# Kernel optimization log

Measured on AMD Instinct MI355X. Metric: run time of the kernel, lower is better.

Reference implementation:

```python
import jax, jax.numpy as jnp
import numpy as np

BS, SEQ, D_IN, D_OUT = 4, 1024, 1024, 1024
N_SKILLS, RANK = 8, 4
SCALING = 1.0  # lora_alpha / rank, folded into one constant
NEG_INF = -1e38


def setup_inputs() -> dict:
    key = jax.random.key(0)
    ks = jax.random.split(key, 5)
    x = jax.random.normal(ks[0], (BS, SEQ, D_IN), jnp.float32)
    phi = jax.random.normal(ks[1], (D_IN, N_SKILLS), jnp.float32) * 0.02
    lora_a = jax.random.normal(ks[2], (N_SKILLS, D_IN, RANK), jnp.float32) * 0.02
    lora_b = jax.random.normal(ks[3], (N_SKILLS, RANK, D_OUT), jnp.float32) * 0.02
    W = jax.random.normal(ks[4], (D_OUT, D_IN), jnp.float32) * 0.02
    b = jnp.zeros((D_OUT,), jnp.float32)
    # left-padded sequences with an instruction prefix right after the padding
    pad_len = np.array([100, 0, 250, 50])
    inst_len = 300
    pad = np.zeros((BS, SEQ), np.int32)
    inst = np.zeros((BS, SEQ), np.int32)
    for i in range(BS):
        pad[i, pad_len[i]:] = 1
        inst[i, pad_len[i]:pad_len[i] + inst_len] = 1
    return {"x": x, "phi": phi, "lora_a": lora_a, "lora_b": lora_b,
            "W": W, "b": b,
            "inst_mask": jnp.asarray(inst), "pad_mask": jnp.asarray(pad)}


def _causal_prefix_mask(inst_mask, pad_mask):
    # faithful port of create_causal_prefix_mask (padding_side='left')
    bs, seq = inst_mask.shape
    first_one = jnp.argmax(inst_mask, axis=1, keepdims=True)          # [b,1]
    n_ones = jnp.sum(inst_mask, axis=1, keepdims=True)                # [b,1]
    thresh = first_one + n_ones                                       # last_one_idx + 1
    exp = jnp.broadcast_to(thresh, (bs, seq))                         # [b,s]
    inv = jnp.maximum(seq - exp - jnp.arange(seq)[None, :], 0)[:, ::-1]
    m = (exp + inv) * pad_mask                                        # [b,s]
    m3 = m[:, :, None] * pad_mask[:, None, :]                         # [b,s,s]
    ar = jnp.arange(seq)[None, None, :]
    return ar < m3                                                    # bool [b,s,s]


def reference(x, phi, lora_a, lora_b, W, b, inst_mask, pad_mask):
    # router: mixing logits per token per skill
    mw = jnp.einsum('bsd,dn->bsn', x, phi)                            # [b,s,k]
    cm = _causal_prefix_mask(inst_mask, pad_mask)                     # [b,s,s]
    padf = pad_mask.astype(x.dtype)
    # expand over attended positions p, mask, softmax over p
    logits = jnp.where(cm[..., None], mw[:, :, None, :], NEG_INF)     # [b,s,p,k]
    logits = jnp.transpose(logits, (0, 3, 1, 2))                      # [b,k,s,p]
    D = jax.nn.softmax(logits, axis=-1)
    D = D * padf[:, None, :, None]                                    # zero padded query rows
    # token mixing: contract over source tokens (last axis of D)
    input_mixed = jnp.einsum('bsd,bkps->bkpd', x, D)                  # [b,k,s,d]
    # per-skill LoRA (n_splits == 1, q squeezed)
    ar_r = jnp.einsum('bksd,kdr->bskr', input_mixed, lora_a)          # [b,s,k,r]
    ad = jnp.einsum('bskr,krd->bskd', ar_r, lora_b)                   # [b,s,k,d_out]
    # softmax-weighted combine over skills
    C = jax.nn.softmax(mw, axis=-1)
    adapter_out = jnp.einsum('bsk,bskd->bsd', C, ad) * SCALING
    base = jnp.einsum('bsd,od->bso', x, W) + b
    return base + adapter_out
```

## Files before the change

kernel.cpp:

```cpp
#include <hip/hip_runtime.h>
#include <hip/hip_bf16.h>
#include <cstdint>

#define SEQ   1024
#define DOUT  1024
#define KDIM  1024
#define MTOT  4096

typedef __bf16 bf16x8 __attribute__((ext_vector_type(8)));
typedef float  f32x4  __attribute__((ext_vector_type(4)));

__device__ inline unsigned short f2bf(float f) {
  union { float f; unsigned u; } a; a.f = f;
  unsigned r = a.u + 0x7fff + ((a.u >> 16) & 1);
  return (unsigned short)(r >> 16);
}

__device__ inline void gl16(const void* g, void* l) {
  __builtin_amdgcn_global_load_lds((__attribute__((address_space(1))) void*)g,
                                   (__attribute__((address_space(3))) void*)l, 16, 0, 0);
}

__global__ __launch_bounds__(256) void k_prep(const float4* __restrict__ x, ushort4* __restrict__ xb,
                                              const float* __restrict__ phi, const float* __restrict__ la,
                                              unsigned short* __restrict__ Wc) {
  int blk = blockIdx.x, tid = threadIdx.x;
  if (blk < 4096) {
    int i = blk * 256 + tid;
    float4 v = x[i];
    ushort4 o; o.x = f2bf(v.x); o.y = f2bf(v.y); o.z = f2bf(v.z); o.w = f2bf(v.w);
    xb[i] = o;
  } else {
    int i = (blk - 4096) * 256 + tid;
    int row = 1024 + (i >> 10), d = i & 1023;
    float v;
    if (row < 1032)       v = phi[d * 8 + (row - 1024)];
    else if (row < 1064)  { int kr = row - 1032; v = la[(kr >> 2) * 4096 + d * 4 + (kr & 3)]; }
    else                  v = 0.f;
    Wc[(size_t)row * 1024 + d] = f2bf(v);
  }
}

__global__ __launch_bounds__(256) void k_mwz(const unsigned short* __restrict__ xb,
                                             const unsigned short* __restrict__ Wc0,
                                             const float* __restrict__ W, const float* __restrict__ lb,
                                             const int* __restrict__ inst,
                                             unsigned short* __restrict__ Wc, unsigned short* __restrict__ B2T,
                                             int* __restrict__ thr, float* __restrict__ mwzP) {
  __shared__ unsigned short As[64 * 32];
  __shared__ unsigned short Bs[48 * 32];
  int blk = blockIdx.x, t = threadIdx.x;
  if (blk >= 256) {
    if (blk < 4352) {
      size_t i = (size_t)(blk - 256) * 256 + t;
      Wc[i] = f2bf(W[i]);
    } else if (blk < 4480) {
      int i = (blk - 4352) * 256 + t;
      int n = i >> 5, kr = i & 31;
      B2T[i] = f2bf(lb[kr * 1024 + n]);
    } else {
      int b = t >> 6, lane = t & 63;
      int fo = 1 << 30, no = 0;
#pragma unroll
      for (int j = 0; j < 16; ++j) {
        int p = j * 64 + lane;
        int iv = inst[b * SEQ + p];
        if (iv > 0) fo = min(fo, p);
        no += iv;
      }
#pragma unroll
      for (int d = 1; d < 64; d <<= 1) { fo = min(fo, __shfl_xor(fo, d)); no += __shfl_xor(no, d); }
      if (lane == 0) thr[b] = (no > 0) ? fo + no : 0;
    }
    return;
  }
  int bm = blk & 63, ks = blk >> 6;
  int wave = t >> 6, lane = t & 63;
  int quad = lane >> 4, lr = lane & 15;
  f32x4 acc[3];
#pragma unroll
  for (int i = 0; i < 3; ++i) acc[i] = (f32x4){0.f, 0.f, 0.f, 0.f};
  const unsigned short* aG = xb + (size_t)bm * 64 * KDIM + ks * 256;
  const unsigned short* bG = Wc0 + (size_t)1024 * KDIM + ks * 256;
  int r0 = t >> 2, c0 = (t & 3) * 8;
  for (int kb = 0; kb < 256; kb += 32) {
    __syncthreads();
    gl16(aG + (size_t)r0 * KDIM + kb + c0, &As[wave * 512]);
    if (t < 192) gl16(bG + (size_t)r0 * KDIM + kb + c0, &Bs[wave * 512]);
    __syncthreads();
    bf16x8 af = *(const bf16x8*)&As[(wave * 16 + lr) * 32 + quad * 8];
#pragma unroll
    for (int ni = 0; ni < 3; ++ni) {
      bf16x8 bfr = *(const bf16x8*)&Bs[(ni * 16 + lr) * 32 + quad * 8];
      acc[ni] = __builtin_amdgcn_mfma_f32_16x16x32_bf16(af, bfr, acc[ni], 0, 0, 0);
    }
  }
#pragma unroll
  for (int ni = 0; ni < 3; ++ni) {
    int c = ni * 16 + lr;
#pragma unroll
    for (int rg = 0; rg < 4; ++rg) {
      int row = bm * 64 + wave * 16 + quad * 4 + rg;
      if (c < 40) mwzP[(size_t)(ks * 40 + c) * MTOT + row] = acc[ni][rg];
    }
  }
}

__global__ __launch_bounds__(1024) void k_scan_gate(const float* __restrict__ mwzP,
                                                    const int* __restrict__ pad, const int* __restrict__ thr,
                                                    unsigned short* __restrict__ gb) {
  int b = blockIdx.x, c = blockIdx.y;
  int tid = threadIdx.x, wv = tid >> 6, lane = tid & 63;
  __shared__ float wsz[16], wsp[16];
  __shared__ float sv, spc;
  int q = b * SEQ + tid;
  float pm = (float)pad[q];
  float z = 0.f;
#pragma unroll
  for (int s = 0; s < 4; ++s) z += mwzP[(size_t)(s * 40 + 8 + c) * MTOT + q];
  z *= pm;
  float vz = z, vp = pm;
#pragma unroll
  for (int d = 1; d < 64; d <<= 1) {
    float oz = __shfl_up(vz, d), op = __shfl_up(vp, d);
    if (lane >= d) { vz += oz; vp += op; }
  }
  if (lane == 63) { wsz[wv] = vz; wsp[wv] = vp; }
  __syncthreads();
  if (wv == 0 && lane < 16) {
    float oz = wsz[lane], op = wsp[lane], sz = oz, sp = op;
#pragma unroll
    for (int d = 1; d < 16; d <<= 1) {
      float tz = __shfl_up(sz, d), tp = __shfl_up(sp, d);
      if (lane >= d) { sz += tz; sp += tp; }
    }
    wsz[lane] = sz - oz; wsp[lane] = sp - op;
  }
  __syncthreads();
  vz += wsz[wv]; vp += wsp[wv];
  int th = thr[b];
  if (th > 0 && tid == th - 1) { sv = vz; spc = vp; }
  __syncthreads();
  unsigned short o = 0;
  if (pm != 0.f) {
    bool own = (tid + 1 >= th);
    float Tv  = own ? vz : sv;
    float cnt = own ? vp : spc;
    float C[8], mx = -1e30f;
#pragma unroll
    for (int k = 0; k < 8; ++k) {
      float m = 0.f;
#pragma unroll
      for (int s = 0; s < 4; ++s) m += mwzP[(size_t)(s * 40 + k) * MTOT + q];
      C[k] = m; mx = fmaxf(mx, m);
    }
    float sm = 0.f;
#pragma unroll
    for (int k = 0; k < 8; ++k) { C[k] = __expf(C[k] - mx); sm += C[k]; }
    o = f2bf(C[c >> 2] * Tv / (sm * cnt));
  }
  gb[(size_t)q * 32 + c] = o;
}

__global__ __launch_bounds__(256) void k_gemm(const unsigned short* __restrict__ A,
                                              const unsigned short* __restrict__ Wc,
                                              const unsigned short* __restrict__ gb,
                                              const unsigned short* __restrict__ B2T,
                                              float* __restrict__ out,
                                              const float* __restrict__ bias) {
  __shared__ __align__(16) unsigned short As[2][128 * 64];
  __shared__ __align__(16) unsigned short Bs[2][64 * 64];
  int bm = blockIdx.x, bn = blockIdx.y;
  int t = threadIdx.x;
  int wave = t >> 6, lane = t & 63;
  int wr = wave >> 1, wc = wave & 1;
  int quad = lane >> 4, lr = lane & 15;
  f32x4 acc[4][2];
#pragma unroll
  for (int i = 0; i < 4; i++)
#pragma unroll
    for (int j = 0; j < 2; j++) acc[i][j] = (f32x4){0.f, 0.f, 0.f, 0.f};

  {
    bf16x8 ga[4], gBf[2];
#pragma unroll
    for (int mi = 0; mi < 4; mi++)
      ga[mi] = *(const bf16x8*)(gb + (size_t)(bm * 128 + wr * 64 + mi * 16 + lr) * 32 + quad * 8);
#pragma unroll
    for (int ni = 0; ni < 2; ni++)
      gBf[ni] = *(const bf16x8*)(B2T + (size_t)(bn * 64 + wc * 32 + ni * 16 + lr) * 32 + quad * 8);
#pragma unroll
    for (int mi = 0; mi < 4; mi++)
#pragma unroll
      for (int ni = 0; ni < 2; ni++)
        acc[mi][ni] = __builtin_amdgcn_mfma_f32_16x16x32_bf16(ga[mi], gBf[ni], acc[mi][ni], 0, 0, 0);
  }

  const unsigned short* aG = A + (size_t)bm * 128 * KDIM;
  const unsigned short* bG = Wc + (size_t)bn * 64 * KDIM;

  auto stage = [&](int b, int kb) {
#pragma unroll
    for (int i = 0; i < 4; ++i) {
      int g = i * 256 + t;
      int r = g >> 3, c = (g & 7) * 8;
      int cs = c ^ ((r & 7) * 8);
      gl16(aG + (size_t)r * KDIM + kb + cs, &As[b][i * 2048 + wave * 512]);
    }
#pragma unroll
    for (int i = 0; i < 2; ++i) {
      int g = i * 256 + t;
      int r = g >> 3, c = (g & 7) * 8;
      int cs = c ^ ((r & 7) * 8);
      gl16(bG + (size_t)r * KDIM + kb + cs, &Bs[b][i * 2048 + wave * 512]);
    }
  };

  stage(0, 0);
  __syncthreads();
  for (int it = 0; it < 16; ++it) {
    int cur = it & 1;
    if (it < 15) stage(cur ^ 1, (it + 1) * 64);
#pragma unroll
    for (int kk = 0; kk < 2; ++kk) {
      bf16x8 af[4], bfr[2];
#pragma unroll
      for (int mi = 0; mi < 4; mi++) {
        int R = wr * 64 + mi * 16 + lr;
        int cc = (kk * 32 + quad * 8) ^ ((R & 7) * 8);
        af[mi] = *(const bf16x8*)&As[cur][R * 64 + cc];
      }
#pragma unroll
      for (int ni = 0; ni < 2; ni++) {
        int R = wc * 32 + ni * 16 + lr;
        int cc = (kk * 32 + quad * 8) ^ ((R & 7) * 8);
        bfr[ni] = *(const bf16x8*)&Bs[cur][R * 64 + cc];
      }
#pragma unroll
      for (int mi = 0; mi < 4; mi++)
#pragma unroll
        for (int ni = 0; ni < 2; ni++)
          acc[mi][ni] = __builtin_amdgcn_mfma_f32_16x16x32_bf16(af[mi], bfr[ni], acc[mi][ni], 0, 0, 0);
    }
    __syncthreads();
  }

#pragma unroll
  for (int mi = 0; mi < 4; mi++) {
#pragma unroll
    for (int ni = 0; ni < 2; ni++) {
      int col = bn * 64 + wc * 32 + ni * 16 + lr;
      float bv = bias[col];
#pragma unroll
      for (int rg = 0; rg < 4; ++rg) {
        int row = bm * 128 + wr * 64 + mi * 16 + quad * 4 + rg;
        out[(size_t)row * DOUT + col] = acc[mi][ni][rg] + bv;
      }
    }
  }
}

extern "C" void kernel_launch(void* const* d_in, const int* in_sizes, int n_in,
                              void* d_out, int out_size, void* d_ws, size_t ws_size,
                              hipStream_t stream) {
  const float* x    = (const float*)d_in[0];
  const float* phi  = (const float*)d_in[1];
  const float* la   = (const float*)d_in[2];
  const float* lb   = (const float*)d_in[3];
  const float* W    = (const float*)d_in[4];
  const float* bias = (const float*)d_in[5];
  const int*   inst = (const int*)d_in[6];
  const int*   pad  = (const int*)d_in[7];
  float* out = (float*)d_out;

  char* ws = (char*)d_ws;
  unsigned short* xb  = (unsigned short*)ws;
  unsigned short* Wc  = (unsigned short*)(ws + 8388608);
  unsigned short* B2T = (unsigned short*)(ws + 10584064);
  float* mwzP = (float*)(ws + 10649600);
  unsigned short* gb  = (unsigned short*)(ws + 13271040);
  int*   thr  = (int*)(ws + 13533184);

  hipLaunchKernelGGL(k_prep,      dim3(4288),   dim3(256),  0, stream,
                     (const float4*)x, (ushort4*)xb, phi, la, Wc);
  hipLaunchKernelGGL(k_mwz,       dim3(4481),   dim3(256),  0, stream,
                     xb, Wc, W, lb, inst, Wc, B2T, thr, mwzP);
  hipLaunchKernelGGL(k_scan_gate, dim3(4, 32),  dim3(1024), 0, stream, mwzP, pad, thr, gb);
  hipLaunchKernelGGL(k_gemm,      dim3(32, 16), dim3(256),  0, stream, xb, Wc, gb, B2T, out, bias);
}
```

Measured before the change: 111.2 us.

## Fold x bf16 conversion into router GEMM and use fine-grained waitcnt barriers

The fp32-to-bf16 conversion of x moves out of the prep kernel. The router GEMM now loads fp32 x directly, converts it in registers and stores it to LDS, so it no longer waits on a prior full conversion pass. Meanwhile extra blocks in the same launch produce xb and the bf16 W. Prep shrinks to the small phi/lora/threshold work. The main GEMM replaces __syncthreads with raw s_barrier plus explicit vmcnt waits so the next stage's loads can stay in flight. The hand-written waitcnt counts are fragile and could cause races if the load count changes.

```diff
diff --git a/kernel.cpp b/kernel.cpp
--- a/kernel.cpp
+++ b/kernel.cpp
@@ -9,6 +9,7 @@
 
 typedef __bf16 bf16x8 __attribute__((ext_vector_type(8)));
 typedef float  f32x4  __attribute__((ext_vector_type(4)));
+typedef unsigned short ushort8v __attribute__((ext_vector_type(8)));
 
 __device__ inline unsigned short f2bf(float f) {
   union { float f; unsigned u; } a; a.f = f;
@@ -21,56 +22,63 @@
                                    (__attribute__((address_space(3))) void*)l, 16, 0, 0);
 }
 
-__global__ __launch_bounds__(256) void k_prep(const float4* __restrict__ x, ushort4* __restrict__ xb,
-                                              const float* __restrict__ phi, const float* __restrict__ la,
-                                              unsigned short* __restrict__ Wc) {
+__device__ inline void barf() {
+  asm volatile("" ::: "memory");
+  __builtin_amdgcn_s_barrier();
+  asm volatile("" ::: "memory");
+}
+
+__global__ __launch_bounds__(256) void k_prep(const float* __restrict__ phi, const float* __restrict__ la,
+                                              const float* __restrict__ lb, const int* __restrict__ inst,
+                                              unsigned short* __restrict__ Wc, unsigned short* __restrict__ B2T,
+                                              int* __restrict__ thr) {
   int blk = blockIdx.x, tid = threadIdx.x;
-  if (blk < 4096) {
+  if (blk < 192) {
     int i = blk * 256 + tid;
-    float4 v = x[i];
-    ushort4 o; o.x = f2bf(v.x); o.y = f2bf(v.y); o.z = f2bf(v.z); o.w = f2bf(v.w);
-    xb[i] = o;
-  } else {
-    int i = (blk - 4096) * 256 + tid;
     int row = 1024 + (i >> 10), d = i & 1023;
     float v;
     if (row < 1032)       v = phi[d * 8 + (row - 1024)];
     else if (row < 1064)  { int kr = row - 1032; v = la[(kr >> 2) * 4096 + d * 4 + (kr & 3)]; }
     else                  v = 0.f;
     Wc[(size_t)row * 1024 + d] = f2bf(v);
-  }
-}
-
-__global__ __launch_bounds__(256) void k_mwz(const unsigned short* __restrict__ xb,
+  } else if (blk < 320) {
+    int i = (blk - 192) * 256 + tid;
+    int n = i >> 5, kr = i & 31;
+    B2T[i] = f2bf(lb[kr * 1024 + n]);
+  } else {
+    int b = tid >> 6, lane = tid & 63;
+    int fo = 1 << 30, no = 0;
+#pragma unroll
+    for (int j = 0; j < 16; ++j) {
+      int p = j * 64 + lane;
+      int iv = inst[b * SEQ + p];
+      if (iv > 0) fo = min(fo, p);
+      no += iv;
+    }
+#pragma unroll
+    for (int d = 1; d < 64; d <<= 1) { fo = min(fo, __shfl_xor(fo, d)); no += __shfl_xor(no, d); }
+    if (lane == 0) thr[b] = (no > 0) ? fo + no : 0;
+  }
+}
+
+__global__ __launch_bounds__(256) void k_mwz(const float* __restrict__ x,
+                                             const float4* __restrict__ x4, ushort4* __restrict__ xb4,
                                              const unsigned short* __restrict__ Wc0,
-                                             const float* __restrict__ W, const float* __restrict__ lb,
-                                             const int* __restrict__ inst,
-                                             unsigned short* __restrict__ Wc, unsigned short* __restrict__ B2T,
-                                             int* __restrict__ thr, float* __restrict__ mwzP) {
-  __shared__ unsigned short As[64 * 32];
-  __shared__ unsigned short Bs[48 * 32];
+                                             const float* __restrict__ W,
+                                             unsigned short* __restrict__ Wc,
+                                             float* __restrict__ mwzP) {
+  __shared__ __align__(16) unsigned short As[64 * 32];
+  __shared__ __align__(16) unsigned short Bs[48 * 32];
   int blk = blockIdx.x, t = threadIdx.x;
   if (blk >= 256) {
     if (blk < 4352) {
       size_t i = (size_t)(blk - 256) * 256 + t;
+      float4 v = x4[i];
+      ushort4 o; o.x = f2bf(v.x); o.y = f2bf(v.y); o.z = f2bf(v.z); o.w = f2bf(v.w);
+      xb4[i] = o;
+    } else {
+      size_t i = (size_t)(blk - 4352) * 256 + t;
       Wc[i] = f2bf(W[i]);
-    } else if (blk < 4480) {
-      int i = (blk - 4352) * 256 + t;
-      int n = i >> 5, kr = i & 31;
-      B2T[i] = f2bf(lb[kr * 1024 + n]);
-    } else {
-      int b = t >> 6, lane = t & 63;
-      int fo = 1 << 30, no = 0;
-#pragma unroll
-      for (int j = 0; j < 16; ++j) {
-        int p = j * 64 + lane;
-        int iv = inst[b * SEQ + p];
-        if (iv > 0) fo = min(fo, p);
-        no += iv;
-      }
-#pragma unroll
-      for (int d = 1; d < 64; d <<= 1) { fo = min(fo, __shfl_xor(fo, d)); no += __shfl_xor(no, d); }
-      if (lane == 0) thr[b] = (no > 0) ? fo + no : 0;
     }
     return;
   }
@@ -80,14 +88,28 @@
   f32x4 acc[3];
 #pragma unroll
   for (int i = 0; i < 3; ++i) acc[i] = (f32x4){0.f, 0.f, 0.f, 0.f};
-  const unsigned short* aG = xb + (size_t)bm * 64 * KDIM + ks * 256;
+  const float* aF = x + (size_t)(bm * 64) * KDIM + ks * 256;
   const unsigned short* bG = Wc0 + (size_t)1024 * KDIM + ks * 256;
   int r0 = t >> 2, c0 = (t & 3) * 8;
+  const float* aP = aF + (size_t)r0 * KDIM + c0;
+  float4 a0 = *(const float4*)(aP);
+  float4 a1 = *(const float4*)(aP + 4);
   for (int kb = 0; kb < 256; kb += 32) {
-    __syncthreads();
-    gl16(aG + (size_t)r0 * KDIM + kb + c0, &As[wave * 512]);
+    barf();
+    ushort8v u;
+    u[0] = f2bf(a0.x); u[1] = f2bf(a0.y); u[2] = f2bf(a0.z); u[3] = f2bf(a0.w);
+    u[4] = f2bf(a1.x); u[5] = f2bf(a1.y); u[6] = f2bf(a1.z); u[7] = f2bf(a1.w);
+    *reinterpret_cast<__shared__ ushort8v*>(&As[t * 8]) = u;
     if (t < 192) gl16(bG + (size_t)r0 * KDIM + kb + c0, &Bs[wave * 512]);
-    __syncthreads();
+    if (kb + 32 < 256) {
+      asm volatile("" ::: "memory");
+      a0 = *(const float4*)(aP + kb + 32);
+      a1 = *(const float4*)(aP + kb + 36);
+      asm volatile("s_waitcnt vmcnt(2) lgkmcnt(0)" ::: "memory");
+    } else {
+      asm volatile("s_waitcnt vmcnt(0) lgkmcnt(0)" ::: "memory");
+    }
+    barf();
     bf16x8 af = *(const bf16x8*)&As[(wave * 16 + lr) * 32 + quad * 8];
 #pragma unroll
     for (int ni = 0; ni < 3; ++ni) {
@@ -217,10 +239,17 @@
   };
 
   stage(0, 0);
-  __syncthreads();
+  asm volatile("s_waitcnt vmcnt(0)" ::: "memory");
+  barf();
   for (int it = 0; it < 16; ++it) {
     int cur = it & 1;
-    if (it < 15) stage(cur ^ 1, (it + 1) * 64);
+    if (it < 15) {
+      stage(cur ^ 1, (it + 1) * 64);
+      asm volatile("s_waitcnt vmcnt(6)" ::: "memory");
+    } else {
+      asm volatile("s_waitcnt vmcnt(0)" ::: "memory");
+    }
+    barf();
 #pragma unroll
     for (int kk = 0; kk < 2; ++kk) {
       bf16x8 af[4], bfr[2];
@@ -242,7 +271,7 @@
         for (int ni = 0; ni < 2; ni++)
           acc[mi][ni] = __builtin_amdgcn_mfma_f32_16x16x32_bf16(af[mi], bfr[ni], acc[mi][ni], 0, 0, 0);
     }
-    __syncthreads();
+    barf();
   }
 
 #pragma unroll
@@ -281,10 +310,10 @@
   unsigned short* gb  = (unsigned short*)(ws + 13271040);
   int*   thr  = (int*)(ws + 13533184);
 
-  hipLaunchKernelGGL(k_prep,      dim3(4288),   dim3(256),  0, stream,
-                     (const float4*)x, (ushort4*)xb, phi, la, Wc);
-  hipLaunchKernelGGL(k_mwz,       dim3(4481),   dim3(256),  0, stream,
-                     xb, Wc, W, lb, inst, Wc, B2T, thr, mwzP);
+  hipLaunchKernelGGL(k_prep,      dim3(321),    dim3(256),  0, stream,
+                     phi, la, lb, inst, Wc, B2T, thr);
+  hipLaunchKernelGGL(k_mwz,       dim3(8448),   dim3(256),  0, stream,
+                     x, (const float4*)x, (ushort4*)xb, Wc, W, Wc, mwzP);
   hipLaunchKernelGGL(k_scan_gate, dim3(4, 32),  dim3(1024), 0, stream, mwzP, pad, thr, gb);
   hipLaunchKernelGGL(k_gemm,      dim3(32, 16), dim3(256),  0, stream, xb, Wc, gb, B2T, out, bias);
 }
```

Result: no change. 111.1 us (-0.1%).
